# Kernel tuning notes

Hardware: AMD Instinct MI355X
Metric: run time of the kernel (lower is better)

The kernel has to match this reference:

```python
import jax, jax.numpy as jnp
import numpy as np

B, LC, LQ, D = 32, 2048, 256, 256


def setup_inputs() -> dict:
    key = jax.random.key(0)
    kc, kq, kcm, kqm, kw = jax.random.split(key, 5)
    context = jax.random.normal(kc, (B, LC, D), dtype=jnp.float32)
    query = jax.random.normal(kq, (B, LQ, D), dtype=jnp.float32)
    # True = masked (matches torch masked_fill semantics)
    context_mask = jax.random.randint(kcm, (B, LC), 0, 2).astype(bool)
    query_mask = jax.random.randint(kqm, (B, LQ), 0, 2).astype(bool)
    # nn.Linear(3*dim, 1, bias=False) weight, flattened to (3D,)
    w0 = jax.random.normal(kw, (3 * D,), dtype=jnp.float32) * (1.0 / np.sqrt(3 * D))
    return {"context": context, "query": query, "context_mask": context_mask,
            "query_mask": query_mask, "w0": w0}


def reference(context, query, context_mask, query_mask, w0):
    d = context.shape[-1]
    wc, wq, wm = w0[:d], w0[d:2 * d], w0[2 * d:]
    # trilinear sim: w0 . [c, q, c*q]  ==  c.wc + q.wq + (c*wm) q^T
    sc = context @ wc                                   # (B, Lc)
    sq = query @ wq                                     # (B, Lq)
    sim = sc[:, :, None] + sq[:, None, :] + jnp.einsum(
        'bcd,bqd->bcq', context * wm, query)            # (B, Lc, Lq)
    mask = context_mask[:, :, None] | query_mask[:, None, :]
    sim = jnp.where(mask, jnp.float32(-1e30), sim)
    S = jax.nn.softmax(sim, axis=-1)                    # row softmax over Lq
    SS = jax.nn.softmax(sim, axis=1)                    # col softmax over Lc
    S = jnp.nan_to_num(S)
    SS = jnp.nan_to_num(SS)
    A = jnp.einsum('bcq,bqd->bcd', S, query)            # (B, Lc, D)
    T = jnp.einsum('bkq,bkd->bqd', SS, context)         # SS^T @ context, (B, Lq, D)
    Bmat = jnp.einsum('bcq,bqd->bcd', S, T)             # (B, Lc, D)
    return (A, Bmat)
```

## Files before the change

kernel.cpp:

```cpp
#include <hip/hip_runtime.h>

#define B_  32
#define LC_ 2048
#define LQ_ 256
#define D_  256
#define NEGH (-30000.0f)

typedef _Float16 f16;
typedef _Float16 f16x4 __attribute__((ext_vector_type(4)));
typedef _Float16 f16x8 __attribute__((ext_vector_type(8)));
typedef float    f32x4 __attribute__((ext_vector_type(4)));

__global__ __launch_bounds__(256) void k_prep(
    const float* __restrict__ ctx, const float* __restrict__ qry,
    const float* __restrict__ w0, f16* __restrict__ ctx16,
    f16* __restrict__ qrywm16, float* __restrict__ sc, float* __restrict__ sq)
{
    const int lane = threadIdx.x & 63;
    const int wave = threadIdx.x >> 6;
    const int row  = blockIdx.x * 4 + wave;
    const int NC = B_ * LC_;
    if (row < NC) {
        float4 v = *(const float4*)(ctx + (long long)row * D_ + lane * 4);
        f16x4 h; h[0] = (f16)v.x; h[1] = (f16)v.y; h[2] = (f16)v.z; h[3] = (f16)v.w;
        *(f16x4*)(ctx16 + (long long)row * D_ + lane * 4) = h;
        float4 wc = *(const float4*)(w0 + lane * 4);
        float s = v.x*wc.x + v.y*wc.y + v.z*wc.z + v.w*wc.w;
        #pragma unroll
        for (int off = 32; off > 0; off >>= 1) s += __shfl_down(s, off, 64);
        if (lane == 0) sc[row] = s;
    } else {
        int r = row - NC;
        float4 v = *(const float4*)(qry + (long long)r * D_ + lane * 4);
        float4 wm = *(const float4*)(w0 + 2 * D_ + lane * 4);
        f16x4 h;
        h[0] = (f16)(v.x * wm.x); h[1] = (f16)(v.y * wm.y);
        h[2] = (f16)(v.z * wm.z); h[3] = (f16)(v.w * wm.w);
        *(f16x4*)(qrywm16 + (long long)r * D_ + lane * 4) = h;
        float4 wq = *(const float4*)(w0 + D_ + lane * 4);
        float s = v.x*wq.x + v.y*wq.y + v.z*wq.z + v.w*wq.w;
        #pragma unroll
        for (int off = 32; off > 0; off >>= 1) s += __shfl_down(s, off, 64);
        if (lane == 0) sq[r] = s;
    }
}

__global__ __launch_bounds__(256) void k_tq(
    const float* __restrict__ in, f16* __restrict__ out)
{
    __shared__ float tile[64 * 65];
    const int b = blockIdx.z;
    const int r0 = blockIdx.x * 64, c0 = blockIdx.y * 64;
    const int t = threadIdx.x;
    const float* ib = in + (long long)b * LQ_ * D_;
    #pragma unroll
    for (int p = 0; p < 4; ++p) {
        int r = (t >> 4) + p * 16;
        int cb = (t & 15) * 4;
        float4 v = *(const float4*)(ib + (long long)(r0 + r) * D_ + c0 + cb);
        tile[r * 65 + cb + 0] = v.x;
        tile[r * 65 + cb + 1] = v.y;
        tile[r * 65 + cb + 2] = v.z;
        tile[r * 65 + cb + 3] = v.w;
    }
    __syncthreads();
    f16* ob = out + (long long)b * 512 * LQ_;
    #pragma unroll
    for (int p = 0; p < 4; ++p) {
        int c = (t >> 4) + p * 16;
        int rb = (t & 15) * 4;
        f16x4 h;
        h[0] = (f16)tile[(rb + 0) * 65 + c];
        h[1] = (f16)tile[(rb + 1) * 65 + c];
        h[2] = (f16)tile[(rb + 2) * 65 + c];
        h[3] = (f16)tile[(rb + 3) * 65 + c];
        *(f16x4*)(ob + (long long)(c0 + c) * LQ_ + r0 + rb) = h;
    }
}

#define LDA1 40
__global__ __launch_bounds__(256) void k_g1(
    const f16* __restrict__ ctx16, const f16* __restrict__ qrywm16,
    const float* __restrict__ sc, const float* __restrict__ sq,
    const int* __restrict__ cmask, const int* __restrict__ qmask,
    f16* __restrict__ sim16,
    float* __restrict__ rowm, float* __restrict__ rowinvl,
    float* __restrict__ pm, float* __restrict__ pl)
{
    __shared__ f16 As[128 * LDA1];
    __shared__ f16 Bs[256 * LDA1];
    __shared__ float rowpm[4][64], rowps[4][64];
    __shared__ float colpm[4][128], colps[4][128];
    __shared__ float rowmax_s[128], colmax_s[256];
    const int b = blockIdx.z;
    const int c0 = blockIdx.x * 128;
    const int t = threadIdx.x, lane = t & 63, wv = t >> 6;
    const int wm_off = (wv >> 1) * 64, wn_off = (wv & 1) * 128;
    const f16* Ab = ctx16 + ((long long)b * LC_ + c0) * D_;
    const f16* Bb = qrywm16 + (long long)b * LQ_ * D_;
    const int srow = t >> 2, scg = (t & 3) * 8;
    f32x4 acc[4][8] = {};
    for (int k0 = 0; k0 < D_; k0 += 32) {
        #pragma unroll
        for (int p = 0; p < 2; ++p) {
            int r = srow + p * 64;
            *(f16x8*)(As + r * LDA1 + scg) = *(const f16x8*)(Ab + (long long)r * D_ + k0 + scg);
        }
        #pragma unroll
        for (int p = 0; p < 4; ++p) {
            int r = srow + p * 64;
            *(f16x8*)(Bs + r * LDA1 + scg) = *(const f16x8*)(Bb + (long long)r * D_ + k0 + scg);
        }
        __syncthreads();
        f16x8 af[4], bf[8];
        #pragma unroll
        for (int i = 0; i < 4; ++i)
            af[i] = *(const f16x8*)(As + (wm_off + i * 16 + (lane & 15)) * LDA1 + (lane >> 4) * 8);
        #pragma unroll
        for (int j = 0; j < 8; ++j)
            bf[j] = *(const f16x8*)(Bs + (wn_off + j * 16 + (lane & 15)) * LDA1 + (lane >> 4) * 8);
        #pragma unroll
        for (int i = 0; i < 4; ++i)
            #pragma unroll
            for (int j = 0; j < 8; ++j)
                acc[i][j] = __builtin_amdgcn_mfma_f32_16x16x32_f16(af[i], bf[j], acc[i][j], 0, 0, 0);
        __syncthreads();
    }
    float sqv[8]; int qmv[8];
    #pragma unroll
    for (int j = 0; j < 8; ++j) {
        int q = wn_off + j * 16 + (lane & 15);
        sqv[j] = sq[b * LQ_ + q];
        qmv[j] = qmask[b * LQ_ + q];
    }
    float scv_[4][4]; int cmv_[4][4];
    #pragma unroll
    for (int i = 0; i < 4; ++i)
        #pragma unroll
        for (int r = 0; r < 4; ++r) {
            int c = c0 + wm_off + i * 16 + (lane >> 4) * 4 + r;
            scv_[i][r] = sc[b * LC_ + c];
            cmv_[i][r] = cmask[b * LC_ + c];
        }
    float rmax[4][4], cmax[8];
    #pragma unroll
    for (int i = 0; i < 4; ++i)
        #pragma unroll
        for (int r = 0; r < 4; ++r) rmax[i][r] = -INFINITY;
    #pragma unroll
    for (int j = 0; j < 8; ++j) cmax[j] = -INFINITY;
    #pragma unroll
    for (int i = 0; i < 4; ++i) {
        #pragma unroll
        for (int r = 0; r < 4; ++r) {
            int c = c0 + wm_off + i * 16 + (lane >> 4) * 4 + r;
            f16* orow = sim16 + ((long long)b * LC_ + c) * LQ_ + wn_off + (lane & 15);
            #pragma unroll
            for (int j = 0; j < 8; ++j) {
                float val = (cmv_[i][r] | qmv[j]) ? NEGH : (acc[i][j][r] + scv_[i][r] + sqv[j]);
                f16 hh = (f16)val;
                orow[j * 16] = hh;
                float vr = (float)hh;
                rmax[i][r] = fmaxf(rmax[i][r], vr);
                cmax[j]    = fmaxf(cmax[j], vr);
            }
        }
    }
    #pragma unroll
    for (int i = 0; i < 4; ++i)
        #pragma unroll
        for (int r = 0; r < 4; ++r) {
            rmax[i][r] = fmaxf(rmax[i][r], __shfl_xor(rmax[i][r], 1, 64));
            rmax[i][r] = fmaxf(rmax[i][r], __shfl_xor(rmax[i][r], 2, 64));
            rmax[i][r] = fmaxf(rmax[i][r], __shfl_xor(rmax[i][r], 4, 64));
            rmax[i][r] = fmaxf(rmax[i][r], __shfl_xor(rmax[i][r], 8, 64));
        }
    #pragma unroll
    for (int j = 0; j < 8; ++j) {
        cmax[j] = fmaxf(cmax[j], __shfl_xor(cmax[j], 16, 64));
        cmax[j] = fmaxf(cmax[j], __shfl_xor(cmax[j], 32, 64));
    }
    if ((lane & 15) == 0) {
        #pragma unroll
        for (int i = 0; i < 4; ++i)
            #pragma unroll
            for (int r = 0; r < 4; ++r)
                rowpm[wv][i * 16 + (lane >> 4) * 4 + r] = rmax[i][r];
    }
    if (lane < 16) {
        #pragma unroll
        for (int j = 0; j < 8; ++j) colpm[wv][j * 16 + lane] = cmax[j];
    }
    __syncthreads();
    if (t < 128)
        rowmax_s[t] = fmaxf(rowpm[2 * (t >> 6)][t & 63], rowpm[2 * (t >> 6) + 1][t & 63]);
    colmax_s[t] = fmaxf(colpm[t >> 7][t & 127], colpm[(t >> 7) + 2][t & 127]);
    __syncthreads();
    float rmf[4][4], cmf[8];
    #pragma unroll
    for (int i = 0; i < 4; ++i)
        #pragma unroll
        for (int r = 0; r < 4; ++r)
            rmf[i][r] = rowmax_s[wm_off + i * 16 + (lane >> 4) * 4 + r];
    #pragma unroll
    for (int j = 0; j < 8; ++j) cmf[j] = colmax_s[wn_off + j * 16 + (lane & 15)];
    float rsum[4][4] = {}, csum[8] = {};
    #pragma unroll
    for (int i = 0; i < 4; ++i) {
        #pragma unroll
        for (int r = 0; r < 4; ++r) {
            #pragma unroll
            for (int j = 0; j < 8; ++j) {
                float val = (cmv_[i][r] | qmv[j]) ? NEGH : (acc[i][j][r] + scv_[i][r] + sqv[j]);
                float vr = (float)(f16)val;
                rsum[i][r] += __expf(vr - rmf[i][r]);
                csum[j]    += __expf(vr - cmf[j]);
            }
        }
    }
    #pragma unroll
    for (int i = 0; i < 4; ++i)
        #pragma unroll
        for (int r = 0; r < 4; ++r) {
            rsum[i][r] += __shfl_xor(rsum[i][r], 1, 64);
            rsum[i][r] += __shfl_xor(rsum[i][r], 2, 64);
            rsum[i][r] += __shfl_xor(rsum[i][r], 4, 64);
            rsum[i][r] += __shfl_xor(rsum[i][r], 8, 64);
        }
    #pragma unroll
    for (int j = 0; j < 8; ++j) {
        csum[j] += __shfl_xor(csum[j], 16, 64);
        csum[j] += __shfl_xor(csum[j], 32, 64);
    }
    if ((lane & 15) == 0) {
        #pragma unroll
        for (int i = 0; i < 4; ++i)
            #pragma unroll
            for (int r = 0; r < 4; ++r)
                rowps[wv][i * 16 + (lane >> 4) * 4 + r] = rsum[i][r];
    }
    if (lane < 16) {
        #pragma unroll
        for (int j = 0; j < 8; ++j) colps[wv][j * 16 + lane] = csum[j];
    }
    __syncthreads();
    if (t < 128) {
        float l = rowps[2 * (t >> 6)][t & 63] + rowps[2 * (t >> 6) + 1][t & 63];
        rowm[b * LC_ + c0 + t]    = rowmax_s[t];
        rowinvl[b * LC_ + c0 + t] = 1.0f / l;
    }
    {
        int idx = (b * 16 + blockIdx.x) * LQ_ + t;
        pm[idx] = colmax_s[t];
        pl[idx] = colps[t >> 7][t & 127] + colps[(t >> 7) + 2][t & 127];
    }
}

__global__ __launch_bounds__(256) void k_colreduce(
    const float* __restrict__ pm, const float* __restrict__ pl,
    float* __restrict__ colm, float* __restrict__ colinvl)
{
    const int col = blockIdx.x * 256 + threadIdx.x;
    const int b = col >> 8, q = col & 255;
    float M = -INFINITY, L = 0.f;
    for (int ch = 0; ch < 16; ++ch) {
        int idx = (b * 16 + ch) * LQ_ + q;
        float m = pm[idx], l = pl[idx];
        float nM = fmaxf(M, m);
        L = L * __expf(M - nM) + l * __expf(m - nM);
        M = nM;
    }
    colm[col] = M; colinvl[col] = 1.0f / L;
}

#define LDA3 66
__global__ __launch_bounds__(256) void k_g3(
    const f16* __restrict__ ctx16, const f16* __restrict__ sim16,
    const float* __restrict__ colm, const float* __restrict__ colinvl,
    f16* __restrict__ Bcat)
{
    __shared__ f16 As[128 * LDA3];
    __shared__ f16 Bs[64 * LDA3];
    __shared__ float colm_s[64], cil_s[64];
    const int b = blockIdx.x;
    const int combo = blockIdx.y;
    const int qt = combo & 3, dh = combo >> 2;
    const int q0 = qt * 64, d0 = dh * 128;
    const int t = threadIdx.x, lane = t & 63, wv = t >> 6;
    const int wm_off = (wv >> 1) * 64, wn_off = (wv & 1) * 32;
    if (t < 64) {
        colm_s[t] = colm[b * LQ_ + q0 + t];
        cil_s[t]  = colinvl[b * LQ_ + q0 + t];
    }
    __syncthreads();
    const f16* Ab = ctx16 + (long long)b * LC_ * D_;
    const f16* Sb = sim16 + (long long)b * LC_ * LQ_;
    f32x4 acc[4][2] = {};
    const int acc_ = t >> 4, ad8 = (t & 15) * 8;
    const int bcc = t >> 3, bq8 = (t & 7) * 8;
    for (int c0 = 0; c0 < LC_; c0 += 64) {
        #pragma unroll
        for (int p = 0; p < 4; ++p) {
            int cc = acc_ + p * 16;
            f16x8 h = *(const f16x8*)(Ab + (long long)(c0 + cc) * D_ + d0 + ad8);
            #pragma unroll
            for (int j = 0; j < 8; ++j)
                As[(ad8 + j) * LDA3 + cc] = h[j];
        }
        #pragma unroll
        for (int p = 0; p < 2; ++p) {
            int cc = bcc + p * 32;
            f16x8 h = *(const f16x8*)(Sb + (long long)(c0 + cc) * LQ_ + q0 + bq8);
            #pragma unroll
            for (int j = 0; j < 8; ++j)
                Bs[(bq8 + j) * LDA3 + cc] = (f16)__expf((float)h[j] - colm_s[bq8 + j]);
        }
        __syncthreads();
        #pragma unroll
        for (int kk = 0; kk < 64; kk += 32) {
            f16x8 af[4], bf[2];
            #pragma unroll
            for (int i = 0; i < 4; ++i)
                af[i] = *(const f16x8*)(As + (wm_off + i * 16 + (lane & 15)) * LDA3 + kk + (lane >> 4) * 8);
            #pragma unroll
            for (int j = 0; j < 2; ++j)
                bf[j] = *(const f16x8*)(Bs + (wn_off + j * 16 + (lane & 15)) * LDA3 + kk + (lane >> 4) * 8);
            #pragma unroll
            for (int i = 0; i < 4; ++i)
                #pragma unroll
                for (int j = 0; j < 2; ++j)
                    acc[i][j] = __builtin_amdgcn_mfma_f32_16x16x32_f16(af[i], bf[j], acc[i][j], 0, 0, 0);
        }
        __syncthreads();
    }
    #pragma unroll
    for (int i = 0; i < 4; ++i) {
        #pragma unroll
        for (int r = 0; r < 4; ++r) {
            int d = d0 + wm_off + i * 16 + (lane >> 4) * 4 + r;
            f16* orow = Bcat + (long long)b * 512 * LQ_ + (long long)(256 + d) * LQ_ + q0 + wn_off + (lane & 15);
            #pragma unroll
            for (int j = 0; j < 2; ++j)
                orow[j * 16] = (f16)(acc[i][j][r] * cil_s[wn_off + j * 16 + (lane & 15)]);
        }
    }
}

__global__ __launch_bounds__(512) void k_g23(
    const f16* __restrict__ sim16, const float* __restrict__ rowm,
    const float* __restrict__ rowinvl, const f16* __restrict__ Bcat,
    float* __restrict__ outA, float* __restrict__ outB)
{
    __shared__ f16 As[256 * LDA1];
    __shared__ f16 Bs[256 * LDA1];
    const int b = blockIdx.z;
    const int c0 = blockIdx.x * 256, n0 = blockIdx.y * 256;
    const int t = threadIdx.x, lane = t & 63, wv = t >> 6;
    const int wm_off = (wv >> 2) * 128;
    const int wn_off = (wv & 3) * 64;
    const f16* Ab = sim16 + ((long long)b * LC_ + c0) * LQ_;
    const f16* Bb = Bcat + ((long long)b * 512 + n0) * LQ_;
    const int srow = t >> 2, scg = (t & 3) * 8;
    float rm[2];
    #pragma unroll
    for (int p = 0; p < 2; ++p) rm[p] = rowm[b * LC_ + c0 + srow + p * 128];
    f32x4 acc[8][4] = {};
    for (int k0 = 0; k0 < LQ_; k0 += 32) {
        #pragma unroll
        for (int p = 0; p < 2; ++p) {
            int r = srow + p * 128;
            f16x8 h = *(const f16x8*)(Ab + (long long)r * LQ_ + k0 + scg);
            f16x8 e;
            #pragma unroll
            for (int j = 0; j < 8; ++j) e[j] = (f16)__expf((float)h[j] - rm[p]);
            *(f16x8*)(As + r * LDA1 + scg) = e;
            *(f16x8*)(Bs + r * LDA1 + scg) = *(const f16x8*)(Bb + (long long)r * LQ_ + k0 + scg);
        }
        __syncthreads();
        f16x8 bf[4];
        #pragma unroll
        for (int j = 0; j < 4; ++j)
            bf[j] = *(const f16x8*)(Bs + (wn_off + j * 16 + (lane & 15)) * LDA1 + (lane >> 4) * 8);
        #pragma unroll
        for (int i = 0; i < 8; ++i) {
            f16x8 af = *(const f16x8*)(As + (wm_off + i * 16 + (lane & 15)) * LDA1 + (lane >> 4) * 8);
            #pragma unroll
            for (int j = 0; j < 4; ++j)
                acc[i][j] = __builtin_amdgcn_mfma_f32_16x16x32_f16(af, bf[j], acc[i][j], 0, 0, 0);
        }
        __syncthreads();
    }
    float* outp = (n0 == 0) ? outA : outB;
    #pragma unroll
    for (int i = 0; i < 8; ++i) {
        #pragma unroll
        for (int r = 0; r < 4; ++r) {
            int c = c0 + wm_off + i * 16 + (lane >> 4) * 4 + r;
            float ri = rowinvl[b * LC_ + c];
            float* orow = outp + ((long long)b * LC_ + c) * D_ + wn_off + (lane & 15);
            #pragma unroll
            for (int j = 0; j < 4; ++j)
                orow[j * 16] = acc[i][j][r] * ri;
        }
    }
}

extern "C" void kernel_launch(void* const* d_in, const int* in_sizes, int n_in,
                              void* d_out, int out_size, void* d_ws, size_t ws_size,
                              hipStream_t stream) {
    const float* ctx   = (const float*)d_in[0];
    const float* qry   = (const float*)d_in[1];
    const int*   cmask = (const int*)d_in[2];
    const int*   qmask = (const int*)d_in[3];
    const float* w0    = (const float*)d_in[4];
    float* out = (float*)d_out;

    char* w = (char*)d_ws;
    float* sc      = (float*)w;  w += (long long)65536 * 4;
    float* sq      = (float*)w;  w += (long long)8192 * 4;
    float* rowm    = (float*)w;  w += (long long)65536 * 4;
    float* rowinvl = (float*)w;  w += (long long)65536 * 4;
    float* colm    = (float*)w;  w += (long long)8192 * 4;
    float* colinvl = (float*)w;  w += (long long)8192 * 4;
    float* pm      = (float*)w;  w += (long long)524288 * 4;
    float* pl      = (float*)w;  w += (long long)524288 * 4;
    f16*   sim16   = (f16*)w;    w += (long long)16777216 * 2;
    f16*   ctx16   = (f16*)w;    w += (long long)16777216 * 2;
    f16*   qrywm16 = (f16*)w;    w += (long long)2097152 * 2;
    f16*   Bcat    = (f16*)w;    w += (long long)4194304 * 2;

    k_prep<<<18432, 256, 0, stream>>>(ctx, qry, w0, ctx16, qrywm16, sc, sq);
    k_tq<<<dim3(4, 4, 32), 256, 0, stream>>>(qry, Bcat);
    k_g1<<<dim3(16, 1, 32), 256, 0, stream>>>(ctx16, qrywm16, sc, sq, cmask, qmask,
        sim16, rowm, rowinvl, pm, pl);
    k_colreduce<<<32, 256, 0, stream>>>(pm, pl, colm, colinvl);
    k_g3<<<dim3(32, 8), 256, 0, stream>>>(ctx16, sim16, colm, colinvl, Bcat);
    k_g23<<<dim3(8, 2, 32), 512, 0, stream>>>(sim16, rowm, rowinvl, Bcat,
        out, out + (long long)B_ * LC_ * D_);
}
```

Baseline: 320.9 us.

## Split-K the T GEMM, add reduce kernel, shrink g23 tiles with register prefetch

The SS^T·context GEMM (k_g3) is split four ways along Lc, so the grid grows from 256 to 1024 blocks. Each split writes fp32 partials, and a new k_bnorm kernel sums them, applies the column normalisation and writes fp16 into Bcat. k_g3 and k_g23 now prefetch the next tile from global memory into registers before each compute step. k_g23 moves from 256x256 tiles with 512 threads to 128x128 tiles with 256 threads, which gives more blocks and fewer registers per thread. The cost is extra partial-sum traffic (about 32MB written and read back) and one more kernel launch.

Result: faster. 309.8 us (-3.4%).

```diff
diff --git a/kernel.cpp b/kernel.cpp
--- a/kernel.cpp
+++ b/kernel.cpp
@@ -274,46 +274,58 @@
 }
 
 #define LDA3 66
+#define G3SPLIT 4
+#define G3CHUNK (LC_ / G3SPLIT)
 __global__ __launch_bounds__(256) void k_g3(
     const f16* __restrict__ ctx16, const f16* __restrict__ sim16,
-    const float* __restrict__ colm, const float* __restrict__ colinvl,
-    f16* __restrict__ Bcat)
+    const float* __restrict__ colm, float* __restrict__ Tpart)
 {
     __shared__ f16 As[128 * LDA3];
     __shared__ f16 Bs[64 * LDA3];
-    __shared__ float colm_s[64], cil_s[64];
+    __shared__ float colm_s[64];
     const int b = blockIdx.x;
     const int combo = blockIdx.y;
     const int qt = combo & 3, dh = combo >> 2;
     const int q0 = qt * 64, d0 = dh * 128;
+    const int cbeg = blockIdx.z * G3CHUNK;
     const int t = threadIdx.x, lane = t & 63, wv = t >> 6;
     const int wm_off = (wv >> 1) * 64, wn_off = (wv & 1) * 32;
-    if (t < 64) {
-        colm_s[t] = colm[b * LQ_ + q0 + t];
-        cil_s[t]  = colinvl[b * LQ_ + q0 + t];
-    }
+    if (t < 64) colm_s[t] = colm[b * LQ_ + q0 + t];
     __syncthreads();
     const f16* Ab = ctx16 + (long long)b * LC_ * D_;
     const f16* Sb = sim16 + (long long)b * LC_ * LQ_;
     f32x4 acc[4][2] = {};
     const int acc_ = t >> 4, ad8 = (t & 15) * 8;
     const int bcc = t >> 3, bq8 = (t & 7) * 8;
-    for (int c0 = 0; c0 < LC_; c0 += 64) {
+    f16x8 ha[4], hb[2];
+    #pragma unroll
+    for (int p = 0; p < 4; ++p)
+        ha[p] = *(const f16x8*)(Ab + (long long)(cbeg + acc_ + p * 16) * D_ + d0 + ad8);
+    #pragma unroll
+    for (int p = 0; p < 2; ++p)
+        hb[p] = *(const f16x8*)(Sb + (long long)(cbeg + bcc + p * 32) * LQ_ + q0 + bq8);
+    for (int c0 = cbeg; c0 < cbeg + G3CHUNK; c0 += 64) {
         #pragma unroll
         for (int p = 0; p < 4; ++p) {
             int cc = acc_ + p * 16;
-            f16x8 h = *(const f16x8*)(Ab + (long long)(c0 + cc) * D_ + d0 + ad8);
             #pragma unroll
             for (int j = 0; j < 8; ++j)
-                As[(ad8 + j) * LDA3 + cc] = h[j];
+                As[(ad8 + j) * LDA3 + cc] = ha[p][j];
         }
         #pragma unroll
         for (int p = 0; p < 2; ++p) {
             int cc = bcc + p * 32;
-            f16x8 h = *(const f16x8*)(Sb + (long long)(c0 + cc) * LQ_ + q0 + bq8);
             #pragma unroll
             for (int j = 0; j < 8; ++j)
-                Bs[(bq8 + j) * LDA3 + cc] = (f16)__expf((float)h[j] - colm_s[bq8 + j]);
+                Bs[(bq8 + j) * LDA3 + cc] = (f16)__expf((float)hb[p][j] - colm_s[bq8 + j]);
+        }
+        if (c0 + 64 < cbeg + G3CHUNK) {
+            #pragma unroll
+            for (int p = 0; p < 4; ++p)
+                ha[p] = *(const f16x8*)(Ab + (long long)(c0 + 64 + acc_ + p * 16) * D_ + d0 + ad8);
+            #pragma unroll
+            for (int p = 0; p < 2; ++p)
+                hb[p] = *(const f16x8*)(Sb + (long long)(c0 + 64 + bcc + p * 32) * LQ_ + q0 + bq8);
         }
         __syncthreads();
         #pragma unroll
@@ -333,71 +345,108 @@
         }
         __syncthreads();
     }
+    float* Tb = Tpart + ((long long)blockIdx.z * B_ + b) * (LQ_ * D_);
     #pragma unroll
     for (int i = 0; i < 4; ++i) {
         #pragma unroll
         for (int r = 0; r < 4; ++r) {
             int d = d0 + wm_off + i * 16 + (lane >> 4) * 4 + r;
-            f16* orow = Bcat + (long long)b * 512 * LQ_ + (long long)(256 + d) * LQ_ + q0 + wn_off + (lane & 15);
+            float* orow = Tb + (long long)d * LQ_ + q0 + wn_off + (lane & 15);
             #pragma unroll
             for (int j = 0; j < 2; ++j)
-                orow[j * 16] = (f16)(acc[i][j][r] * cil_s[wn_off + j * 16 + (lane & 15)]);
-        }
-    }
-}
-
-__global__ __launch_bounds__(512) void k_g23(
+                orow[j * 16] = acc[i][j][r];
+        }
+    }
+}
+
+__global__ __launch_bounds__(256) void k_bnorm(
+    const float* __restrict__ Tpart, const float* __restrict__ colinvl,
+    f16* __restrict__ Bcat)
+{
+    const long long i4 = ((long long)blockIdx.x * 256 + threadIdx.x) * 4;
+    const int q = (int)(i4 & 255);
+    const int d = (int)((i4 >> 8) & 255);
+    const int b = (int)(i4 >> 16);
+    float4 s = *(const float4*)(Tpart + i4);
+    #pragma unroll
+    for (int p = 1; p < G3SPLIT; ++p) {
+        float4 v = *(const float4*)(Tpart + (long long)p * (B_ * LQ_ * D_) + i4);
+        s.x += v.x; s.y += v.y; s.z += v.z; s.w += v.w;
+    }
+    float4 ci = *(const float4*)(colinvl + b * LQ_ + q);
+    f16x4 h;
+    h[0] = (f16)(s.x * ci.x); h[1] = (f16)(s.y * ci.y);
+    h[2] = (f16)(s.z * ci.z); h[3] = (f16)(s.w * ci.w);
+    *(f16x4*)(Bcat + (long long)b * 512 * LQ_ + (long long)(256 + d) * LQ_ + q) = h;
+}
+
+__global__ __launch_bounds__(256) void k_g23(
     const f16* __restrict__ sim16, const float* __restrict__ rowm,
     const float* __restrict__ rowinvl, const f16* __restrict__ Bcat,
     float* __restrict__ outA, float* __restrict__ outB)
 {
-    __shared__ f16 As[256 * LDA1];
-    __shared__ f16 Bs[256 * LDA1];
+    __shared__ f16 As[128 * LDA1];
+    __shared__ f16 Bs[128 * LDA1];
     const int b = blockIdx.z;
-    const int c0 = blockIdx.x * 256, n0 = blockIdx.y * 256;
+    const int c0 = blockIdx.x * 128, n0 = blockIdx.y * 128;
     const int t = threadIdx.x, lane = t & 63, wv = t >> 6;
-    const int wm_off = (wv >> 2) * 128;
-    const int wn_off = (wv & 3) * 64;
+    const int wm_off = (wv >> 1) * 64, wn_off = (wv & 1) * 64;
     const f16* Ab = sim16 + ((long long)b * LC_ + c0) * LQ_;
     const f16* Bb = Bcat + ((long long)b * 512 + n0) * LQ_;
     const int srow = t >> 2, scg = (t & 3) * 8;
     float rm[2];
     #pragma unroll
-    for (int p = 0; p < 2; ++p) rm[p] = rowm[b * LC_ + c0 + srow + p * 128];
-    f32x4 acc[8][4] = {};
+    for (int p = 0; p < 2; ++p) rm[p] = rowm[b * LC_ + c0 + srow + p * 64];
+    f32x4 acc[4][4] = {};
+    f16x8 ha[2], hb[2];
+    #pragma unroll
+    for (int p = 0; p < 2; ++p) {
+        int r = srow + p * 64;
+        ha[p] = *(const f16x8*)(Ab + (long long)r * LQ_ + scg);
+        hb[p] = *(const f16x8*)(Bb + (long long)r * LQ_ + scg);
+    }
     for (int k0 = 0; k0 < LQ_; k0 += 32) {
         #pragma unroll
         for (int p = 0; p < 2; ++p) {
-            int r = srow + p * 128;
-            f16x8 h = *(const f16x8*)(Ab + (long long)r * LQ_ + k0 + scg);
+            int r = srow + p * 64;
             f16x8 e;
             #pragma unroll
-            for (int j = 0; j < 8; ++j) e[j] = (f16)__expf((float)h[j] - rm[p]);
+            for (int j = 0; j < 8; ++j) e[j] = (f16)__expf((float)ha[p][j] - rm[p]);
             *(f16x8*)(As + r * LDA1 + scg) = e;
-            *(f16x8*)(Bs + r * LDA1 + scg) = *(const f16x8*)(Bb + (long long)r * LQ_ + k0 + scg);
-        }
-        __syncthreads();
-        f16x8 bf[4];
+            *(f16x8*)(Bs + r * LDA1 + scg) = hb[p];
+        }
+        if (k0 + 32 < LQ_) {
+            #pragma unroll
+            for (int p = 0; p < 2; ++p) {
+                int r = srow + p * 64;
+                ha[p] = *(const f16x8*)(Ab + (long long)r * LQ_ + k0 + 32 + scg);
+                hb[p] = *(const f16x8*)(Bb + (long long)r * LQ_ + k0 + 32 + scg);
+            }
+        }
+        __syncthreads();
+        f16x8 af[4], bf[4];
+        #pragma unroll
+        for (int i = 0; i < 4; ++i)
+            af[i] = *(const f16x8*)(As + (wm_off + i * 16 + (lane & 15)) * LDA1 + (lane >> 4) * 8);
         #pragma unroll
         for (int j = 0; j < 4; ++j)
             bf[j] = *(const f16x8*)(Bs + (wn_off + j * 16 + (lane & 15)) * LDA1 + (lane >> 4) * 8);
         #pragma unroll
-        for (int i = 0; i < 8; ++i) {
-            f16x8 af = *(const f16x8*)(As + (wm_off + i * 16 + (lane & 15)) * LDA1 + (lane >> 4) * 8);
+        for (int i = 0; i < 4; ++i)
             #pragma unroll
             for (int j = 0; j < 4; ++j)
-                acc[i][j] = __builtin_amdgcn_mfma_f32_16x16x32_f16(af, bf[j], acc[i][j], 0, 0, 0);
-        }
-        __syncthreads();
-    }
-    float* outp = (n0 == 0) ? outA : outB;
-    #pragma unroll
-    for (int i = 0; i < 8; ++i) {
+                acc[i][j] = __builtin_amdgcn_mfma_f32_16x16x32_f16(af[i], bf[j], acc[i][j], 0, 0, 0);
+        __syncthreads();
+    }
+    float* outp = (n0 < 256) ? outA : outB;
+    const int nbase = (n0 < 256) ? n0 : (n0 - 256);
+    #pragma unroll
+    for (int i = 0; i < 4; ++i) {
         #pragma unroll
         for (int r = 0; r < 4; ++r) {
             int c = c0 + wm_off + i * 16 + (lane >> 4) * 4 + r;
             float ri = rowinvl[b * LC_ + c];
-            float* orow = outp + ((long long)b * LC_ + c) * D_ + wn_off + (lane & 15);
+            float* orow = outp + ((long long)b * LC_ + c) * D_ + nbase + wn_off + (lane & 15);
             #pragma unroll
             for (int j = 0; j < 4; ++j)
                 orow[j * 16] = acc[i][j][r] * ri;
@@ -428,13 +477,15 @@
     f16*   ctx16   = (f16*)w;    w += (long long)16777216 * 2;
     f16*   qrywm16 = (f16*)w;    w += (long long)2097152 * 2;
     f16*   Bcat    = (f16*)w;    w += (long long)4194304 * 2;
+    float* Tpart   = (float*)w;  w += (long long)G3SPLIT * 2097152 * 4;
 
     k_prep<<<18432, 256, 0, stream>>>(ctx, qry, w0, ctx16, qrywm16, sc, sq);
     k_tq<<<dim3(4, 4, 32), 256, 0, stream>>>(qry, Bcat);
     k_g1<<<dim3(16, 1, 32), 256, 0, stream>>>(ctx16, qrywm16, sc, sq, cmask, qmask,
         sim16, rowm, rowinvl, pm, pl);
     k_colreduce<<<32, 256, 0, stream>>>(pm, pl, colm, colinvl);
-    k_g3<<<dim3(32, 8), 256, 0, stream>>>(ctx16, sim16, colm, colinvl, Bcat);
-    k_g23<<<dim3(8, 2, 32), 512, 0, stream>>>(sim16, rowm, rowinvl, Bcat,
+    k_g3<<<dim3(32, 8, G3SPLIT), 256, 0, stream>>>(ctx16, sim16, colm, Tpart);
+    k_bnorm<<<2048, 256, 0, stream>>>(Tpart, colinvl, Bcat);
+    k_g23<<<dim3(16, 4, 32), 256, 0, stream>>>(sim16, rowm, rowinvl, Bcat,
         out, out + (long long)B_ * LC_ * D_);
 }
```
